# Optimization experiments

Hardware: AMD Instinct MI355X
Metric: run time of the kernel (lower is better)

Reference implementation:

```python
import jax, jax.numpy as jnp
import numpy as np

N_NODES = 12000
N_EDGES = 384000
F_IN = 128       # num_features
D = 64           # latent_dim (hidden_dim), num_gc_layers = 1
H_DEC = 64       # ceil(F_IN / 2)
BN_EPS = 1e-4


def _gcn_conv(x, W, b, src, dst, n):
    # PyG GCNConv: h = x @ W; add self-loops; sym-normalized scatter-add; + bias
    h = x @ W
    loop = jnp.arange(n)
    s = jnp.concatenate([src, loop])
    d = jnp.concatenate([dst, loop])
    deg = jax.ops.segment_sum(jnp.ones(s.shape[0], dtype=x.dtype), d, num_segments=n)
    dis = jax.lax.rsqrt(deg)  # deg >= 1 thanks to self-loops
    norm = dis[s] * dis[d]    # [E+N]
    out = jax.ops.segment_sum(h[s] * norm[:, None], d, num_segments=n)
    return out + b


def _bn_train(x, gamma, beta):
    # BatchNorm1d, training-mode batch statistics, biased variance, eps=1e-4
    mu = jnp.mean(x, axis=0)
    xc = x - mu
    var = jnp.mean(xc * xc, axis=0)
    return xc * jax.lax.rsqrt(var + BN_EPS) * gamma + beta


def _enc_layer(x, W, b, g, be, src, dst, n):
    # GCNConv -> Sigmoid -> (dropout no-op) -> BatchNorm
    return _bn_train(jax.nn.sigmoid(_gcn_conv(x, W, b, src, dst, n)), g, be)


def setup_inputs() -> dict:
    key = jax.random.key(0)
    ks = jax.random.split(key, 16)
    inp = {
        'x': jax.random.normal(ks[0], (N_NODES, F_IN), dtype=jnp.float32),
        'src': jax.random.randint(ks[1], (N_EDGES,), 0, N_NODES),
        'dst': jax.random.randint(ks[2], (N_EDGES,), 0, N_NODES),
        'batch': jnp.zeros((N_NODES,), dtype=jnp.int32),
        'noise': jax.random.normal(ks[3], (N_NODES, D), dtype=jnp.float32),
        # base_gcn encoder (GCNConv F_IN -> D, BN)
        'W0': jax.random.normal(ks[4], (F_IN, D), dtype=jnp.float32) * 0.08,
        'b0': jnp.zeros((D,), dtype=jnp.float32),
        'g0': jnp.ones((D,), dtype=jnp.float32),
        'be0': jnp.zeros((D,), dtype=jnp.float32),
        # gcn_mean encoder (GCNConv D -> D, BN)
        'Wm': jax.random.normal(ks[5], (D, D), dtype=jnp.float32) * 0.12,
        'bm': jnp.zeros((D,), dtype=jnp.float32),
        'gm': jnp.ones((D,), dtype=jnp.float32),
        'bem': jnp.zeros((D,), dtype=jnp.float32),
        # gcn_logstddev encoder (GCNConv D -> D, BN)
        'Ws': jax.random.normal(ks[6], (D, D), dtype=jnp.float32) * 0.12,
        'bs': jnp.zeros((D,), dtype=jnp.float32),
        'gs': jnp.ones((D,), dtype=jnp.float32),
        'bes': jnp.zeros((D,), dtype=jnp.float32),
        # decoder MLP: Linear(D, H_DEC) -> LeakyReLU -> Linear(H_DEC, F_IN)
        'Dw1': jax.random.normal(ks[7], (D, H_DEC), dtype=jnp.float32) * 0.12,
        'Db1': jnp.zeros((H_DEC,), dtype=jnp.float32),
        'Dw2': jax.random.normal(ks[8], (H_DEC, F_IN), dtype=jnp.float32) * 0.12,
        'Db2': jnp.zeros((F_IN,), dtype=jnp.float32),
    }
    return inp


def reference(x, src, dst, batch, noise,
              W0, b0, g0, be0,
              Wm, bm, gm, bem,
              Ws, bs, gs, bes,
              Dw1, Db1, Dw2, Db2):
    n = x.shape[0]
    hidden = _enc_layer(x, W0, b0, g0, be0, src, dst, n)          # [N, D]
    mean = _enc_layer(hidden, Wm, bm, gm, bem, src, dst, n)       # [N, D]
    logstd = _enc_layer(hidden, Ws, bs, gs, bes, src, dst, n)     # [N, D]
    z = noise * jnp.exp(logstd) + mean                            # reparam trick
    # decoder MLP (LeakyReLU default slope 0.01)
    h = jax.nn.leaky_relu(z @ Dw1 + Db1, negative_slope=0.01)
    reconstructed_x = h @ Dw2 + Db2                               # [N, F_IN]
    A_pred = jax.nn.sigmoid(z @ z.T)                              # [N, N]
    return (reconstructed_x, A_pred)
```

## Files before the change

### kernel.cpp

```cpp
#include <hip/hip_runtime.h>
#include <hip/hip_bf16.h>

#define N_NODES 12000
#define N_EDGES 384000
#define F_INN   128
#define DLAT    64
#define BN_EPS  1e-4f

__device__ __forceinline__ float sigmoidf(float x) { return 1.0f / (1.0f + __expf(-x)); }

__global__ void k_init(int* cnt, int* cur, int n) {
    int i = blockIdx.x * blockDim.x + threadIdx.x;
    if (i < n) { cnt[i] = 0; cur[i] = 0; }
}

__global__ void k_count(const int* dst, int* cnt, int e) {
    int i = blockIdx.x * blockDim.x + threadIdx.x;
    if (i < e) atomicAdd(&cnt[dst[i]], 1);
}

__global__ void k_scan(const int* cnt, int* offs, int n) {
    __shared__ int buf[1024];
    __shared__ int carry;
    int tid = threadIdx.x;
    if (tid == 0) { carry = 0; offs[0] = 0; }
    __syncthreads();
    for (int base = 0; base < n; base += 1024) {
        int i = base + tid;
        int v = (i < n) ? cnt[i] : 0;
        buf[tid] = v;
        __syncthreads();
        for (int o = 1; o < 1024; o <<= 1) {
            int t = (tid >= o) ? buf[tid - o] : 0;
            __syncthreads();
            buf[tid] += t;
            __syncthreads();
        }
        if (i < n) offs[i + 1] = carry + buf[tid];
        __syncthreads();
        if (tid == 0) carry += buf[1023];
        __syncthreads();
    }
}

__global__ void k_dis(const int* cnt, float* dis, int n) {
    int i = blockIdx.x * blockDim.x + threadIdx.x;
    if (i < n) dis[i] = rsqrtf((float)(cnt[i] + 1));
}

__global__ void k_scatter(const int* src, const int* dst, const int* offs, int* cur,
                          int* ssrc, int e) {
    int i = blockIdx.x * blockDim.x + threadIdx.x;
    if (i < e) {
        int d = dst[i];
        int p = atomicAdd(&cur[d], 1);
        ssrc[offs[d] + p] = src[i];
    }
}

__global__ void k_mm(const float* __restrict__ X, int n, int K,
                     const float* __restrict__ Wa, int Ma,
                     const float* __restrict__ Wb, int Mb,
                     float* __restrict__ out) {
    __shared__ float Wl[8192];
    int M = Ma + Mb;
    for (int idx = threadIdx.x; idx < K * M; idx += blockDim.x) {
        int k = idx / M, m = idx % M;
        Wl[idx] = (m < Ma) ? Wa[k * Ma + m] : Wb[k * Mb + (m - Ma)];
    }
    __syncthreads();
    int rpb = blockDim.x / M;
    int r = blockIdx.x * rpb + threadIdx.x / M;
    int m = threadIdx.x % M;
    if (r >= n) return;
    const float* xr = X + (size_t)r * K;
    float acc = 0.f;
    for (int k = 0; k < K; k++) acc += xr[k] * Wl[k * M + m];
    out[(size_t)r * M + m] = acc;
}

__global__ void k_agg(const float* __restrict__ h, const float* __restrict__ dis,
                      const int* __restrict__ offs, const int* __restrict__ ssrc,
                      const float* __restrict__ ba, const float* __restrict__ bb, int Ma,
                      float* __restrict__ out, int dim, int n) {
    int t = blockIdx.x * blockDim.x + threadIdx.x;
    int node = t / dim;
    if (node >= n) return;
    int f = t - node * dim;
    float di = dis[node];
    float acc = h[(size_t)node * dim + f] * di;
    int e0 = offs[node], e1 = offs[node + 1];
    int j = e0;
    for (; j + 3 < e1; j += 4) {
        int s0 = ssrc[j], s1 = ssrc[j + 1], s2 = ssrc[j + 2], s3 = ssrc[j + 3];
        acc += h[(size_t)s0 * dim + f] * dis[s0];
        acc += h[(size_t)s1 * dim + f] * dis[s1];
        acc += h[(size_t)s2 * dim + f] * dis[s2];
        acc += h[(size_t)s3 * dim + f] * dis[s3];
    }
    for (; j < e1; j++) {
        int s = ssrc[j];
        acc += h[(size_t)s * dim + f] * dis[s];
    }
    float bias = (f < Ma) ? ba[f] : bb[f - Ma];
    out[(size_t)node * dim + f] = sigmoidf(acc * di + bias);
}

__global__ void k_stats(const float* __restrict__ act, int dim, int n,
                        float* __restrict__ mu, float* __restrict__ var) {
    int c = blockIdx.x;
    float s = 0.f, s2 = 0.f;
    for (int r = threadIdx.x; r < n; r += blockDim.x) {
        float v = act[(size_t)r * dim + c];
        s += v; s2 += v * v;
    }
    __shared__ float sh[512];
    sh[threadIdx.x] = s; sh[256 + threadIdx.x] = s2;
    __syncthreads();
    for (int o = 128; o > 0; o >>= 1) {
        if (threadIdx.x < o) {
            sh[threadIdx.x] += sh[threadIdx.x + o];
            sh[256 + threadIdx.x] += sh[256 + threadIdx.x + o];
        }
        __syncthreads();
    }
    if (threadIdx.x == 0) {
        float m = sh[0] / n;
        mu[c] = m;
        var[c] = sh[256] / n - m * m;
    }
}

__global__ void k_bnapply(const float* __restrict__ in, float* __restrict__ out,
                          const float* __restrict__ mu, const float* __restrict__ var,
                          const float* __restrict__ g, const float* __restrict__ be,
                          int dim, size_t total) {
    size_t i = (size_t)blockIdx.x * blockDim.x + threadIdx.x;
    if (i >= total) return;
    int f = (int)(i % dim);
    out[i] = (in[i] - mu[f]) * rsqrtf(var[f] + BN_EPS) * g[f] + be[f];
}

__global__ void k_z(const float* __restrict__ act2, const float* __restrict__ noise,
                    const float* __restrict__ mu, const float* __restrict__ var,
                    const float* __restrict__ gm, const float* __restrict__ bem,
                    const float* __restrict__ gs, const float* __restrict__ bes,
                    float* __restrict__ z, int n) {
    int i = blockIdx.x * blockDim.x + threadIdx.x;
    if (i >= n * DLAT) return;
    int row = i >> 6, j = i & 63;
    const float* ar = act2 + (size_t)row * 128;
    float m  = (ar[j]      - mu[j])      * rsqrtf(var[j]      + BN_EPS) * gm[j] + bem[j];
    float ls = (ar[j + 64] - mu[j + 64]) * rsqrtf(var[j + 64] + BN_EPS) * gs[j] + bes[j];
    z[i] = noise[i] * __expf(ls) + m;
}

__global__ void k_dec(const float* __restrict__ z,
                      const float* __restrict__ W1, const float* __restrict__ B1,
                      const float* __restrict__ W2, const float* __restrict__ B2,
                      float* __restrict__ out, int n) {
    __shared__ float w1[64 * 64];
    __shared__ float w2[64 * 128];
    __shared__ float hl[4 * 64];
    for (int i = threadIdx.x; i < 4096; i += 256) w1[i] = W1[i];
    for (int i = threadIdx.x; i < 8192; i += 256) w2[i] = W2[i];
    __syncthreads();
    int r0 = blockIdx.x * 4;
    {
        int r = threadIdx.x / 64, hc = threadIdx.x % 64;
        int row = r0 + r;
        float acc = B1[hc];
        const float* zr = z + (size_t)row * 64;
        for (int k = 0; k < 64; k++) acc += zr[k] * w1[k * 64 + hc];
        hl[r * 64 + hc] = acc > 0.f ? acc : 0.01f * acc;
    }
    __syncthreads();
    for (int pass = 0; pass < 2; pass++) {
        int r = pass * 2 + threadIdx.x / 128;
        int oc = threadIdx.x % 128;
        int row = r0 + r;
        float acc = B2[oc];
        for (int k = 0; k < 64; k++) acc += hl[r * 64 + k] * w2[k * 128 + oc];
        out[(size_t)row * 128 + oc] = acc;
    }
}

#define TN 188
__global__ __launch_bounds__(256) void k_apred(const float* __restrict__ z,
                                               float* __restrict__ out, int n) {
    __shared__ float zi[4096];
    __shared__ float zj[4096];
    int bi = blockIdx.x % TN, bj = blockIdx.x / TN;
    int i0 = bi * 64, j0 = bj * 64;
    int t = threadIdx.x;
    int lr = t >> 2, kq = t & 3;
    {
        int row = i0 + lr;
        const float4* s = (const float4*)(z + (size_t)row * 64 + kq * 16);
        float4 v0, v1, v2, v3;
        if (row < n) { v0 = s[0]; v1 = s[1]; v2 = s[2]; v3 = s[3]; }
        else { v0 = v1 = v2 = v3 = make_float4(0.f, 0.f, 0.f, 0.f); }
        int k0 = kq * 16;
        float4 vs[4] = {v0, v1, v2, v3};
        for (int q = 0; q < 4; q++) {
            int k = k0 + q * 4;
            zi[(k + 0) * 64 + lr] = vs[q].x;
            zi[(k + 1) * 64 + lr] = vs[q].y;
            zi[(k + 2) * 64 + lr] = vs[q].z;
            zi[(k + 3) * 64 + lr] = vs[q].w;
        }
    }
    {
        int row = j0 + lr;
        const float4* s = (const float4*)(z + (size_t)row * 64 + kq * 16);
        float4 v0, v1, v2, v3;
        if (row < n) { v0 = s[0]; v1 = s[1]; v2 = s[2]; v3 = s[3]; }
        else { v0 = v1 = v2 = v3 = make_float4(0.f, 0.f, 0.f, 0.f); }
        int k0 = kq * 16;
        float4 vs[4] = {v0, v1, v2, v3};
        for (int q = 0; q < 4; q++) {
            int k = k0 + q * 4;
            zj[(k + 0) * 64 + lr] = vs[q].x;
            zj[(k + 1) * 64 + lr] = vs[q].y;
            zj[(k + 2) * 64 + lr] = vs[q].z;
            zj[(k + 3) * 64 + lr] = vs[q].w;
        }
    }
    __syncthreads();

    int tx = t & 15, ty = t >> 4;
    int c0 = tx * 4, r0 = ty * 4;
    float acc[4][4] = {};
    for (int k = 0; k < 64; k++) {
        float4 a = *(const float4*)&zi[k * 64 + r0];
        float4 b = *(const float4*)&zj[k * 64 + c0];
        acc[0][0] += a.x * b.x; acc[0][1] += a.x * b.y; acc[0][2] += a.x * b.z; acc[0][3] += a.x * b.w;
        acc[1][0] += a.y * b.x; acc[1][1] += a.y * b.y; acc[1][2] += a.y * b.z; acc[1][3] += a.y * b.w;
        acc[2][0] += a.z * b.x; acc[2][1] += a.z * b.y; acc[2][2] += a.z * b.z; acc[2][3] += a.z * b.w;
        acc[3][0] += a.w * b.x; acc[3][1] += a.w * b.y; acc[3][2] += a.w * b.z; acc[3][3] += a.w * b.w;
    }
    int col = j0 + c0;
    if (col < n) {
        for (int i = 0; i < 4; i++) {
            int row = i0 + r0 + i;
            if (row >= n) break;
            float4 o;
            o.x = sigmoidf(acc[i][0]);
            o.y = sigmoidf(acc[i][1]);
            o.z = sigmoidf(acc[i][2]);
            o.w = sigmoidf(acc[i][3]);
            *(float4*)&out[(size_t)row * n + col] = o;
        }
    }
}

extern "C" void kernel_launch(void* const* d_in, const int* in_sizes, int n_in,
                              void* d_out, int out_size, void* d_ws, size_t ws_size,
                              hipStream_t stream) {
    const float* x     = (const float*)d_in[0];
    const int*   src   = (const int*)d_in[1];
    const int*   dst   = (const int*)d_in[2];
    const float* noise = (const float*)d_in[4];
    const float* W0  = (const float*)d_in[5];
    const float* b0  = (const float*)d_in[6];
    const float* g0  = (const float*)d_in[7];
    const float* be0 = (const float*)d_in[8];
    const float* Wm  = (const float*)d_in[9];
    const float* bm  = (const float*)d_in[10];
    const float* gm  = (const float*)d_in[11];
    const float* bem = (const float*)d_in[12];
    const float* Ws  = (const float*)d_in[13];
    const float* bs  = (const float*)d_in[14];
    const float* gs  = (const float*)d_in[15];
    const float* bes = (const float*)d_in[16];
    const float* Dw1 = (const float*)d_in[17];
    const float* Db1 = (const float*)d_in[18];
    const float* Dw2 = (const float*)d_in[19];
    const float* Db2 = (const float*)d_in[20];
    float* out = (float*)d_out;

    const int n = N_NODES, e = N_EDGES;

    int*   cnt  = (int*)d_ws;
    int*   offs = (int*)d_ws + 12032;
    int*   cur  = (int*)d_ws + 24064;
    int*   ssrc = (int*)d_ws + 36096;
    float* dis  = (float*)d_ws + 420096;
    float* mu   = (float*)d_ws + 432128;
    float* var  = (float*)d_ws + 432384;
    float* bufA = (float*)d_ws + 432640;
    float* bufB = bufA + (size_t)N_NODES * 128;
    float* zbuf = bufB;

    k_init<<<(n + 255) / 256, 256, 0, stream>>>(cnt, cur, n);
    k_count<<<(e + 255) / 256, 256, 0, stream>>>(dst, cnt, e);
    k_scan<<<1, 1024, 0, stream>>>(cnt, offs, n);
    k_dis<<<(n + 255) / 256, 256, 0, stream>>>(cnt, dis, n);
    k_scatter<<<(e + 255) / 256, 256, 0, stream>>>(src, dst, offs, cur, ssrc, e);

    k_mm<<<n / 4, 256, 0, stream>>>(x, n, F_INN, W0, DLAT, nullptr, 0, bufA);
    k_agg<<<(n * DLAT) / 256, 256, 0, stream>>>(bufA, dis, offs, ssrc, b0, nullptr, DLAT,
                                                bufB, DLAT, n);
    k_stats<<<DLAT, 256, 0, stream>>>(bufB, DLAT, n, mu, var);
    k_bnapply<<<(n * DLAT) / 256, 256, 0, stream>>>(bufB, bufA, mu, var, g0, be0, DLAT,
                                                    (size_t)n * DLAT);

    k_mm<<<n / 2, 256, 0, stream>>>(bufA, n, DLAT, Wm, DLAT, Ws, DLAT, bufB);
    k_agg<<<(n * 128) / 256, 256, 0, stream>>>(bufB, dis, offs, ssrc, bm, bs, DLAT,
                                               bufA, 128, n);
    k_stats<<<128, 256, 0, stream>>>(bufA, 128, n, mu, var);

    k_z<<<(n * DLAT) / 256, 256, 0, stream>>>(bufA, noise, mu, var, gm, bem, gs, bes,
                                              zbuf, n);

    k_dec<<<n / 4, 256, 0, stream>>>(zbuf, Dw1, Db1, Dw2, Db2, out, n);

    k_apred<<<TN * TN, 256, 0, stream>>>(zbuf, out + (size_t)n * F_INN, n);
}
```

Measured before the change: 1.122 ms.

## Exploit symmetry in A_pred, enlarge tiles, and parallelize scan, stats, decoder

The z·zᵀ kernel now uses 128x128 tiles with 8x8 register blocking and computes only upper-triangular tile pairs, mirroring each result into the transposed block so the dot products are done once per pair. The single-block scan now uses wavefront shuffles and also computes the degree normalisation, which removes the separate dis kernel. BatchNorm statistics become a two-stage multi-block reduction instead of one block per column. The decoder processes 16 rows per block to reuse the weights loaded into shared memory. The mirrored stores are column-strided across rows, which may reduce write coalescing on the 576MB output, and that write is the dominant cost.

```diff
diff --git a/kernel.cpp b/kernel.cpp
--- a/kernel.cpp
+++ b/kernel.cpp
@@ -19,33 +19,42 @@
     if (i < e) atomicAdd(&cnt[dst[i]], 1);
 }
 
-__global__ void k_scan(const int* cnt, int* offs, int n) {
-    __shared__ int buf[1024];
-    __shared__ int carry;
+__global__ void k_scan(const int* __restrict__ cnt, int* __restrict__ offs,
+                       float* __restrict__ dis, int n) {
+    __shared__ int wsum[16];
     int tid = threadIdx.x;
-    if (tid == 0) { carry = 0; offs[0] = 0; }
-    __syncthreads();
-    for (int base = 0; base < n; base += 1024) {
-        int i = base + tid;
-        int v = (i < n) ? cnt[i] : 0;
-        buf[tid] = v;
-        __syncthreads();
-        for (int o = 1; o < 1024; o <<= 1) {
-            int t = (tid >= o) ? buf[tid - o] : 0;
-            __syncthreads();
-            buf[tid] += t;
-            __syncthreads();
-        }
-        if (i < n) offs[i + 1] = carry + buf[tid];
-        __syncthreads();
-        if (tid == 0) carry += buf[1023];
-        __syncthreads();
-    }
-}
-
-__global__ void k_dis(const int* cnt, float* dis, int n) {
-    int i = blockIdx.x * blockDim.x + threadIdx.x;
-    if (i < n) dis[i] = rsqrtf((float)(cnt[i] + 1));
+    int base = tid * 12;
+    int v[12];
+    int s = 0;
+#pragma unroll
+    for (int q = 0; q < 12; q++) {
+        int i = base + q;
+        v[q] = (i < n) ? cnt[i] : 0;
+        s += v[q];
+        if (i < n) dis[i] = rsqrtf((float)(v[q] + 1));
+    }
+    int lane = tid & 63, w = tid >> 6;
+    int ps = s;
+#pragma unroll
+    for (int o = 1; o < 64; o <<= 1) {
+        int t2 = __shfl_up(ps, o, 64);
+        if (lane >= o) ps += t2;
+    }
+    if (lane == 63) wsum[w] = ps;
+    __syncthreads();
+    if (tid == 0) {
+        int acc = 0;
+        for (int i = 0; i < 16; i++) { int t2 = wsum[i]; wsum[i] = acc; acc += t2; }
+    }
+    __syncthreads();
+    int acc = wsum[w] + ps - s;
+#pragma unroll
+    for (int q = 0; q < 12; q++) {
+        int i = base + q;
+        if (i < n) offs[i] = acc;
+        acc += v[q];
+        if (i == n - 1) offs[n] = acc;
+    }
 }
 
 __global__ void k_scatter(const int* src, const int* dst, const int* offs, int* cur,
@@ -106,29 +115,42 @@
     out[(size_t)node * dim + f] = sigmoidf(acc * di + bias);
 }
 
-__global__ void k_stats(const float* __restrict__ act, int dim, int n,
-                        float* __restrict__ mu, float* __restrict__ var) {
-    int c = blockIdx.x;
+#define STATS_BLOCKS 64
+__global__ void k_stats1(const float* __restrict__ act, int dim, int n,
+                         float* __restrict__ part) {
+    int rpb = 256 / dim;
+    int c = threadIdx.x % dim;
+    int rloc = threadIdx.x / dim;
     float s = 0.f, s2 = 0.f;
-    for (int r = threadIdx.x; r < n; r += blockDim.x) {
+    for (int r = blockIdx.x * rpb + rloc; r < n; r += STATS_BLOCKS * rpb) {
         float v = act[(size_t)r * dim + c];
         s += v; s2 += v * v;
     }
     __shared__ float sh[512];
     sh[threadIdx.x] = s; sh[256 + threadIdx.x] = s2;
     __syncthreads();
-    for (int o = 128; o > 0; o >>= 1) {
-        if (threadIdx.x < o) {
-            sh[threadIdx.x] += sh[threadIdx.x + o];
-            sh[256 + threadIdx.x] += sh[256 + threadIdx.x + o];
-        }
-        __syncthreads();
-    }
-    if (threadIdx.x == 0) {
-        float m = sh[0] / n;
-        mu[c] = m;
-        var[c] = sh[256] / n - m * m;
-    }
+    if (rloc == 0) {
+        for (int q = 1; q < rpb; q++) {
+            s += sh[q * dim + c];
+            s2 += sh[256 + q * dim + c];
+        }
+        part[(size_t)(blockIdx.x * dim + c) * 2] = s;
+        part[(size_t)(blockIdx.x * dim + c) * 2 + 1] = s2;
+    }
+}
+
+__global__ void k_stats2(const float* __restrict__ part, int dim, int n,
+                         float* __restrict__ mu, float* __restrict__ var) {
+    int c = threadIdx.x;
+    if (c >= dim) return;
+    float s = 0.f, s2 = 0.f;
+    for (int q = 0; q < STATS_BLOCKS; q++) {
+        s += part[(size_t)(q * dim + c) * 2];
+        s2 += part[(size_t)(q * dim + c) * 2 + 1];
+    }
+    float m = s / n;
+    mu[c] = m;
+    var[c] = s2 / n - m * m;
 }
 
 __global__ void k_bnapply(const float* __restrict__ in, float* __restrict__ out,
@@ -161,95 +183,135 @@
                       float* __restrict__ out, int n) {
     __shared__ float w1[64 * 64];
     __shared__ float w2[64 * 128];
-    __shared__ float hl[4 * 64];
-    for (int i = threadIdx.x; i < 4096; i += 256) w1[i] = W1[i];
-    for (int i = threadIdx.x; i < 8192; i += 256) w2[i] = W2[i];
-    __syncthreads();
-    int r0 = blockIdx.x * 4;
+    __shared__ float zl[16 * 64];
+    __shared__ float hl[16 * 64];
+    int t = threadIdx.x;
+    int row0 = blockIdx.x * 16;
     {
-        int r = threadIdx.x / 64, hc = threadIdx.x % 64;
-        int row = r0 + r;
-        float acc = B1[hc];
-        const float* zr = z + (size_t)row * 64;
-        for (int k = 0; k < 64; k++) acc += zr[k] * w1[k * 64 + hc];
-        hl[r * 64 + hc] = acc > 0.f ? acc : 0.01f * acc;
-    }
-    __syncthreads();
-    for (int pass = 0; pass < 2; pass++) {
-        int r = pass * 2 + threadIdx.x / 128;
-        int oc = threadIdx.x % 128;
-        int row = r0 + r;
-        float acc = B2[oc];
-        for (int k = 0; k < 64; k++) acc += hl[r * 64 + k] * w2[k * 128 + oc];
-        out[(size_t)row * 128 + oc] = acc;
-    }
-}
-
-#define TN 188
-__global__ __launch_bounds__(256) void k_apred(const float* __restrict__ z,
-                                               float* __restrict__ out, int n) {
-    __shared__ float zi[4096];
-    __shared__ float zj[4096];
-    int bi = blockIdx.x % TN, bj = blockIdx.x / TN;
-    int i0 = bi * 64, j0 = bj * 64;
+        const float4* W14 = (const float4*)W1;
+        const float4* W24 = (const float4*)W2;
+        for (int i = t; i < 1024; i += 256) ((float4*)w1)[i] = W14[i];
+        for (int i = t; i < 2048; i += 256) ((float4*)w2)[i] = W24[i];
+        ((float4*)zl)[t] = ((const float4*)(z + (size_t)row0 * 64))[t];
+    }
+    __syncthreads();
+    {
+        int hc = t & 63, rg = t >> 6;
+        float a0 = B1[hc], a1 = a0, a2 = a0, a3 = a0;
+        int rb = rg * 4;
+        for (int k = 0; k < 64; k++) {
+            float wv = w1[k * 64 + hc];
+            a0 += zl[(rb + 0) * 64 + k] * wv;
+            a1 += zl[(rb + 1) * 64 + k] * wv;
+            a2 += zl[(rb + 2) * 64 + k] * wv;
+            a3 += zl[(rb + 3) * 64 + k] * wv;
+        }
+        hl[(rb + 0) * 64 + hc] = a0 > 0.f ? a0 : 0.01f * a0;
+        hl[(rb + 1) * 64 + hc] = a1 > 0.f ? a1 : 0.01f * a1;
+        hl[(rb + 2) * 64 + hc] = a2 > 0.f ? a2 : 0.01f * a2;
+        hl[(rb + 3) * 64 + hc] = a3 > 0.f ? a3 : 0.01f * a3;
+    }
+    __syncthreads();
+    {
+        int oc = t & 127, rg = t >> 7;
+        float o[8];
+#pragma unroll
+        for (int i = 0; i < 8; i++) o[i] = B2[oc];
+        int rb = rg * 8;
+        for (int k = 0; k < 64; k++) {
+            float wv = w2[k * 128 + oc];
+#pragma unroll
+            for (int i = 0; i < 8; i++) o[i] += hl[(rb + i) * 64 + k] * wv;
+        }
+#pragma unroll
+        for (int i = 0; i < 8; i++)
+            out[(size_t)(row0 + rb + i) * 128 + oc] = o[i];
+    }
+}
+
+#define TN2 94
+__global__ __launch_bounds__(256, 2) void k_apred(const float* __restrict__ z,
+                                                  float* __restrict__ out, int n) {
+    __shared__ float zi[64 * 128];
+    __shared__ float zj[64 * 128];
+    int b = blockIdx.x;
+    float ff = (float)(2 * TN2 + 1);
+    int bi = (int)((ff - sqrtf(ff * ff - 8.0f * (float)b)) * 0.5f);
+    while (bi > 0 && b < bi * TN2 - bi * (bi - 1) / 2) bi--;
+    while (b >= (bi + 1) * TN2 - (bi + 1) * bi / 2) bi++;
+    int bj = bi + (b - (bi * TN2 - bi * (bi - 1) / 2));
+    int i0 = bi * 128, j0 = bj * 128;
+
     int t = threadIdx.x;
-    int lr = t >> 2, kq = t & 3;
+    int r = t >> 1, half = t & 1;
     {
-        int row = i0 + lr;
-        const float4* s = (const float4*)(z + (size_t)row * 64 + kq * 16);
-        float4 v0, v1, v2, v3;
-        if (row < n) { v0 = s[0]; v1 = s[1]; v2 = s[2]; v3 = s[3]; }
-        else { v0 = v1 = v2 = v3 = make_float4(0.f, 0.f, 0.f, 0.f); }
-        int k0 = kq * 16;
-        float4 vs[4] = {v0, v1, v2, v3};
-        for (int q = 0; q < 4; q++) {
-            int k = k0 + q * 4;
-            zi[(k + 0) * 64 + lr] = vs[q].x;
-            zi[(k + 1) * 64 + lr] = vs[q].y;
-            zi[(k + 2) * 64 + lr] = vs[q].z;
-            zi[(k + 3) * 64 + lr] = vs[q].w;
-        }
-    }
-    {
-        int row = j0 + lr;
-        const float4* s = (const float4*)(z + (size_t)row * 64 + kq * 16);
-        float4 v0, v1, v2, v3;
-        if (row < n) { v0 = s[0]; v1 = s[1]; v2 = s[2]; v3 = s[3]; }
-        else { v0 = v1 = v2 = v3 = make_float4(0.f, 0.f, 0.f, 0.f); }
-        int k0 = kq * 16;
-        float4 vs[4] = {v0, v1, v2, v3};
-        for (int q = 0; q < 4; q++) {
-            int k = k0 + q * 4;
-            zj[(k + 0) * 64 + lr] = vs[q].x;
-            zj[(k + 1) * 64 + lr] = vs[q].y;
-            zj[(k + 2) * 64 + lr] = vs[q].z;
-            zj[(k + 3) * 64 + lr] = vs[q].w;
+        int row = i0 + r;
+        const float4* s4 = (const float4*)(z + (size_t)row * 64 + half * 32);
+#pragma unroll
+        for (int q = 0; q < 8; q++) {
+            float4 v = (row < n) ? s4[q] : make_float4(0.f, 0.f, 0.f, 0.f);
+            int k = half * 32 + q * 4;
+            zi[(k + 0) * 128 + r] = v.x;
+            zi[(k + 1) * 128 + r] = v.y;
+            zi[(k + 2) * 128 + r] = v.z;
+            zi[(k + 3) * 128 + r] = v.w;
+        }
+        row = j0 + r;
+        const float4* s4b = (const float4*)(z + (size_t)row * 64 + half * 32);
+#pragma unroll
+        for (int q = 0; q < 8; q++) {
+            float4 v = (row < n) ? s4b[q] : make_float4(0.f, 0.f, 0.f, 0.f);
+            int k = half * 32 + q * 4;
+            zj[(k + 0) * 128 + r] = v.x;
+            zj[(k + 1) * 128 + r] = v.y;
+            zj[(k + 2) * 128 + r] = v.z;
+            zj[(k + 3) * 128 + r] = v.w;
         }
     }
     __syncthreads();
 
     int tx = t & 15, ty = t >> 4;
-    int c0 = tx * 4, r0 = ty * 4;
-    float acc[4][4] = {};
+    int c0 = tx * 8, r0 = ty * 8;
+    float acc[8][8] = {};
     for (int k = 0; k < 64; k++) {
-        float4 a = *(const float4*)&zi[k * 64 + r0];
-        float4 b = *(const float4*)&zj[k * 64 + c0];
-        acc[0][0] += a.x * b.x; acc[0][1] += a.x * b.y; acc[0][2] += a.x * b.z; acc[0][3] += a.x * b.w;
-        acc[1][0] += a.y * b.x; acc[1][1] += a.y * b.y; acc[1][2] += a.y * b.z; acc[1][3] += a.y * b.w;
-        acc[2][0] += a.z * b.x; acc[2][1] += a.z * b.y; acc[2][2] += a.z * b.z; acc[2][3] += a.z * b.w;
-        acc[3][0] += a.w * b.x; acc[3][1] += a.w * b.y; acc[3][2] += a.w * b.z; acc[3][3] += a.w * b.w;
-    }
-    int col = j0 + c0;
-    if (col < n) {
-        for (int i = 0; i < 4; i++) {
-            int row = i0 + r0 + i;
-            if (row >= n) break;
-            float4 o;
-            o.x = sigmoidf(acc[i][0]);
-            o.y = sigmoidf(acc[i][1]);
-            o.z = sigmoidf(acc[i][2]);
-            o.w = sigmoidf(acc[i][3]);
-            *(float4*)&out[(size_t)row * n + col] = o;
+        float4 a0 = *(const float4*)&zi[k * 128 + r0];
+        float4 a1 = *(const float4*)&zi[k * 128 + r0 + 4];
+        float4 b0 = *(const float4*)&zj[k * 128 + c0];
+        float4 b1 = *(const float4*)&zj[k * 128 + c0 + 4];
+        float av[8] = {a0.x, a0.y, a0.z, a0.w, a1.x, a1.y, a1.z, a1.w};
+        float bv[8] = {b0.x, b0.y, b0.z, b0.w, b1.x, b1.y, b1.z, b1.w};
+#pragma unroll
+        for (int i = 0; i < 8; i++)
+#pragma unroll
+            for (int j = 0; j < 8; j++) acc[i][j] += av[i] * bv[j];
+    }
+#pragma unroll
+    for (int i = 0; i < 8; i++)
+#pragma unroll
+        for (int j = 0; j < 8; j++) acc[i][j] = sigmoidf(acc[i][j]);
+
+#pragma unroll
+    for (int i = 0; i < 8; i++) {
+        int row = i0 + r0 + i;
+        if (row >= n) continue;
+        if (j0 + c0 + 4 <= n)
+            *(float4*)&out[(size_t)row * n + j0 + c0] =
+                make_float4(acc[i][0], acc[i][1], acc[i][2], acc[i][3]);
+        if (j0 + c0 + 8 <= n)
+            *(float4*)&out[(size_t)row * n + j0 + c0 + 4] =
+                make_float4(acc[i][4], acc[i][5], acc[i][6], acc[i][7]);
+    }
+    if (bi != bj) {
+#pragma unroll
+        for (int j = 0; j < 8; j++) {
+            int row = j0 + c0 + j;
+            if (row >= n) continue;
+            if (i0 + r0 + 4 <= n)
+                *(float4*)&out[(size_t)row * n + i0 + r0] =
+                    make_float4(acc[0][j], acc[1][j], acc[2][j], acc[3][j]);
+            if (i0 + r0 + 8 <= n)
+                *(float4*)&out[(size_t)row * n + i0 + r0 + 4] =
+                    make_float4(acc[4][j], acc[5][j], acc[6][j], acc[7][j]);
         }
     }
 }
@@ -288,32 +350,34 @@
     float* dis  = (float*)d_ws + 420096;
     float* mu   = (float*)d_ws + 432128;
     float* var  = (float*)d_ws + 432384;
-    float* bufA = (float*)d_ws + 432640;
+    float* part = (float*)d_ws + 432640;
+    float* bufA = (float*)d_ws + 449024;
     float* bufB = bufA + (size_t)N_NODES * 128;
     float* zbuf = bufB;
 
     k_init<<<(n + 255) / 256, 256, 0, stream>>>(cnt, cur, n);
     k_count<<<(e + 255) / 256, 256, 0, stream>>>(dst, cnt, e);
-    k_scan<<<1, 1024, 0, stream>>>(cnt, offs, n);
-    k_dis<<<(n + 255) / 256, 256, 0, stream>>>(cnt, dis, n);
+    k_scan<<<1, 1024, 0, stream>>>(cnt, offs, dis, n);
     k_scatter<<<(e + 255) / 256, 256, 0, stream>>>(src, dst, offs, cur, ssrc, e);
 
     k_mm<<<n / 4, 256, 0, stream>>>(x, n, F_INN, W0, DLAT, nullptr, 0, bufA);
     k_agg<<<(n * DLAT) / 256, 256, 0, stream>>>(bufA, dis, offs, ssrc, b0, nullptr, DLAT,
                                                 bufB, DLAT, n);
-    k_stats<<<DLAT, 256, 0, stream>>>(bufB, DLAT, n, mu, var);
+    k_stats1<<<STATS_BLOCKS, 256, 0, stream>>>(bufB, DLAT, n, part);
+    k_stats2<<<1, 64, 0, stream>>>(part, DLAT, n, mu, var);
     k_bnapply<<<(n * DLAT) / 256, 256, 0, stream>>>(bufB, bufA, mu, var, g0, be0, DLAT,
                                                     (size_t)n * DLAT);
 
     k_mm<<<n / 2, 256, 0, stream>>>(bufA, n, DLAT, Wm, DLAT, Ws, DLAT, bufB);
     k_agg<<<(n * 128) / 256, 256, 0, stream>>>(bufB, dis, offs, ssrc, bm, bs, DLAT,
                                                bufA, 128, n);
-    k_stats<<<128, 256, 0, stream>>>(bufA, 128, n, mu, var);
+    k_stats1<<<STATS_BLOCKS, 256, 0, stream>>>(bufA, 128, n, part);
+    k_stats2<<<1, 128, 0, stream>>>(part, 128, n, mu, var);
 
     k_z<<<(n * DLAT) / 256, 256, 0, stream>>>(bufA, noise, mu, var, gm, bem, gs, bes,
                                               zbuf, n);
 
-    k_dec<<<n / 4, 256, 0, stream>>>(zbuf, Dw1, Db1, Dw2, Db2, out, n);
-
-    k_apred<<<TN * TN, 256, 0, stream>>>(zbuf, out + (size_t)n * F_INN, n);
-}
+    k_dec<<<n / 16, 256, 0, stream>>>(zbuf, Dw1, Db1, Dw2, Db2, out, n);
+
+    k_apred<<<TN2 * (TN2 + 1) / 2, 256, 0, stream>>>(zbuf, out + (size_t)n * F_INN, n);
+}
```

Result: faster. 1.007 ms (-10.2%).
